# Performance work log

Hardware: AMD Instinct MI355X
Metric: run time of the kernel (lower is better)

The kernel has to match this reference:

```python
import jax, jax.numpy as jnp
import numpy as np

NUM_HEADS = 8
D_MODEL = 128
MAX_LEN = 500  # RelativePositionalEncoding default


def setup_inputs() -> dict:
    key = jax.random.key(0)
    ks = jax.random.split(key, 13)
    B, S, D = 4, 1024, D_MODEL
    d = {
        'query': jax.random.normal(ks[0], (B, S, D), jnp.float32),
        'key': jax.random.normal(ks[1], (B, S, D), jnp.float32),
        'value': jax.random.normal(ks[2], (B, S, D), jnp.float32),
        # nn.Linear weights stored as (out, in), bias (out,)
        'Wq': jax.random.normal(ks[3], (D, D), jnp.float32) * 0.05,
        'bq': jax.random.normal(ks[4], (D,), jnp.float32) * 0.05,
        'Wk': jax.random.normal(ks[5], (D, D), jnp.float32) * 0.05,
        'bk': jax.random.normal(ks[6], (D,), jnp.float32) * 0.05,
        'Wv': jax.random.normal(ks[7], (D, D), jnp.float32) * 0.05,
        'bv': jax.random.normal(ks[8], (D,), jnp.float32) * 0.05,
        'Wo': jax.random.normal(ks[9], (D, D), jnp.float32) * 0.05,
        'bo': jax.random.normal(ks[10], (D,), jnp.float32) * 0.05,
        # embeddings_table: (2*max_len+1, d_model)
        'emb_table': jax.random.normal(ks[11], (2 * MAX_LEN + 1, D), jnp.float32) * 0.05,
    }
    return d


def reference(query, key, value, Wq, bq, Wk, bk, Wv, bv, Wo, bo, emb_table):
    B, S, D = query.shape
    H = NUM_HEADS
    hd = D // H

    def proj(x, W, b):
        # nn.Linear: x @ W.T + b, then split heads -> [B,H,S,hd]
        return (x @ W.T + b).reshape(B, S, H, hd).transpose(0, 2, 1, 3)

    Q = proj(query, Wq, bq)
    K = proj(key, Wk, bk)
    V = proj(value, Wv, bv)

    scores = jnp.einsum('bhqd,bhkd->bhqk', Q, K) / jnp.sqrt(jnp.float32(hd))

    # relative position bias: table gather (S,S,D) -> (S,S,H,hd);
    # batch dim of the torch expand is redundant, so contract directly.
    r = jnp.arange(S)
    rel_idx = jnp.clip(r[None, :] - r[:, None], -MAX_LEN, MAX_LEN) + MAX_LEN  # (S,S)
    E = emb_table[rel_idx].reshape(S, S, H, hd)  # (q,k,h,d)
    scores = scores + jnp.einsum('bhqd,qkhd->bhqk', Q, E)

    attn = jax.nn.softmax(scores + 1e-9, axis=-1)
    out = jnp.einsum('bhqk,bhkd->bhqd', attn, V)
    out = out.transpose(0, 2, 1, 3).reshape(B, S, D)
    return out @ Wo.T + bo
```

## Files before the change

### kernel.cpp

```cpp
#include <hip/hip_runtime.h>

#define NH 8
#define HD 16
#define SLEN 1024
#define BATCH 4
#define MAXL 500
#define NSEG 4
#define KTILES_PER_SEG 8

typedef float f32x4  __attribute__((ext_vector_type(4)));
typedef float f32x16 __attribute__((ext_vector_type(16)));
typedef short s16x8  __attribute__((ext_vector_type(8)));

__device__ inline ushort f2bf(float f) {
    uint u = __builtin_bit_cast(uint, f);
    u = (u + 0x7fffu + ((u >> 16) & 1u)) >> 16;
    return (ushort)u;
}
__device__ inline float bf2f(ushort h) {
    uint u = ((uint)h) << 16;
    return __builtin_bit_cast(float, u);
}

__global__ __launch_bounds__(256) void emb2bf(const float* __restrict__ emb,
                                              ushort* __restrict__ emb_bf)
{
    int idx = blockIdx.x * 256 + threadIdx.x;
    int e0 = idx * 8;
    if (e0 >= (2 * MAXL + 1) * 128) return;
    const float4 a = *(const float4*)&emb[e0];
    const float4 b = *(const float4*)&emb[e0 + 4];
    ushort tmp[8] = {f2bf(a.x), f2bf(a.y), f2bf(a.z), f2bf(a.w),
                     f2bf(b.x), f2bf(b.y), f2bf(b.z), f2bf(b.w)};
    *(s16x8*)&emb_bf[e0] = *(const s16x8*)tmp;
}

__global__ __launch_bounds__(256) void qkv_proj_mfma(
    const float* __restrict__ xq, const float* __restrict__ xk, const float* __restrict__ xv,
    const float* __restrict__ Wq, const float* __restrict__ bq,
    const float* __restrict__ Wk, const float* __restrict__ bk,
    const float* __restrict__ Wv, const float* __restrict__ bv,
    ushort* __restrict__ Qh, ushort* __restrict__ Kh, ushort* __restrict__ Vt)
{
    const int mode = blockIdx.y;
    const float* x  = (mode == 0) ? xq : (mode == 1) ? xk : xv;
    const float* W  = (mode == 0) ? Wq : (mode == 1) ? Wk : Wv;
    const float* bb = (mode == 0) ? bq : (mode == 1) ? bk : bv;

    __shared__ __align__(16) ushort Xs[64][40];
    __shared__ __align__(16) ushort Ws[128][40];

    const int t = threadIdx.x;
    const int wid = t >> 6, lane = t & 63;
    const int m0 = blockIdx.x * 64;

    f32x4 acc[4][2];
    #pragma unroll
    for (int i = 0; i < 4; ++i)
        #pragma unroll
        for (int j = 0; j < 2; ++j)
            #pragma unroll
            for (int r = 0; r < 4; ++r) acc[i][j][r] = 0.f;

    for (int k0 = 0; k0 < 128; k0 += 32) {
        __syncthreads();
        {
            int m = t >> 2, kb = (t & 3) * 8;
            const float* src = &x[(size_t)(m0 + m) * 128 + k0 + kb];
            const float4 a = *(const float4*)src;
            const float4 b4 = *(const float4*)(src + 4);
            ushort tmp[8] = {f2bf(a.x),f2bf(a.y),f2bf(a.z),f2bf(a.w),
                             f2bf(b4.x),f2bf(b4.y),f2bf(b4.z),f2bf(b4.w)};
            *(s16x8*)&Xs[m][kb] = *(const s16x8*)tmp;
        }
        {
            int n = t >> 1, kb = (t & 1) * 16;
            const float* src = &W[(size_t)n * 128 + k0 + kb];
            ushort tmp[16];
            #pragma unroll
            for (int i = 0; i < 16; ++i) tmp[i] = f2bf(src[i]);
            *(s16x8*)&Ws[n][kb]     = *(const s16x8*)&tmp[0];
            *(s16x8*)&Ws[n][kb + 8] = *(const s16x8*)&tmp[8];
        }
        __syncthreads();
        s16x8 af[4], bf[2];
        #pragma unroll
        for (int ms = 0; ms < 4; ++ms)
            af[ms] = *(const s16x8*)&Xs[16*ms + (lane & 15)][8 * (lane >> 4)];
        #pragma unroll
        for (int ns = 0; ns < 2; ++ns)
            bf[ns] = *(const s16x8*)&Ws[32*wid + 16*ns + (lane & 15)][8 * (lane >> 4)];
        #pragma unroll
        for (int ms = 0; ms < 4; ++ms)
            #pragma unroll
            for (int ns = 0; ns < 2; ++ns)
                acc[ms][ns] = __builtin_amdgcn_mfma_f32_16x16x32_bf16(af[ms], bf[ns], acc[ms][ns], 0, 0, 0);
    }

    const float scale = (mode == 1) ? 0.25f : 1.0f;
    const int b = m0 >> 10;
    #pragma unroll
    for (int ns = 0; ns < 2; ++ns) {
        const int n = 32*wid + 16*ns + (lane & 15);
        const int hh = n >> 4, d = n & 15;
        const float bias = bb[n];
        #pragma unroll
        for (int ms = 0; ms < 4; ++ms) {
            if (mode == 2) {
                ushort4 pk;
                pk.x = f2bf(acc[ms][ns][0] + bias);
                pk.y = f2bf(acc[ms][ns][1] + bias);
                pk.z = f2bf(acc[ms][ns][2] + bias);
                pk.w = f2bf(acc[ms][ns][3] + bias);
                int s0 = (m0 & 1023) + 16*ms + (lane >> 4) * 4;
                *(ushort4*)&Vt[((size_t)((b*8 + hh)*16 + d)) * SLEN + s0] = pk;
            } else {
                ushort* dst = (mode == 0) ? Qh : Kh;
                #pragma unroll
                for (int r = 0; r < 4; ++r) {
                    int mm = m0 + 16*ms + (lane >> 4) * 4 + r;
                    int s = mm & 1023;
                    float v = (acc[ms][ns][r] + bias) * scale;
                    dst[((size_t)(b*8 + hh) * SLEN + s) * HD + d] = f2bf(v);
                }
            }
        }
    }
}

__global__ __launch_bounds__(256) void attn_mfma(
    const ushort* __restrict__ Qh, const ushort* __restrict__ Kh,
    const ushort* __restrict__ Vtg, const ushort* __restrict__ emb_bf,
    float* __restrict__ mp, float* __restrict__ lp, float* __restrict__ op)
{
    __shared__ __align__(16) ushort Kt[32][24];
    __shared__ __align__(16) ushort Vt[16][40];
    __shared__ __align__(16) ushort Eb[160][24];
    __shared__ __align__(16) ushort Pl[4][32][40];
    __shared__ __align__(16) ushort Rl[4][64][36];
    __shared__ float scb[4][32];

    const int tid = threadIdx.x;
    const int wid = tid >> 6, lane = tid & 63;
    const int hi = lane >> 5, q = lane & 31;
    const int bh = blockIdx.y, h = bh & 7;
    const int q0b = blockIdx.x * 128;
    const int q0w = q0b + wid * 32;
    const int seg = blockIdx.z;

    const s16x8 qf = *(const s16x8*)&Qh[((size_t)bh * SLEN + q0w + q) * HD + 8 * hi];

    f32x4 o0, o1;
    #pragma unroll
    for (int r = 0; r < 4; ++r) { o0[r] = 0.f; o1[r] = 0.f; }
    float m = -1e30f, l = 0.f;

    for (int kt = seg * KTILES_PER_SEG; kt < (seg + 1) * KTILES_PER_SEG; ++kt) {
        const int k0 = kt * 32;
        __syncthreads();
        {
            int e = tid * 2, r = e >> 4, d0 = e & 15;
            *(ushort2*)&Kt[r][d0] = *(const ushort2*)&Kh[((size_t)bh * SLEN + k0 + r) * HD + d0];
        }
        {
            int d = tid >> 4, kk = (tid & 15) * 2;
            *(ushort2*)&Vt[d][kk] = *(const ushort2*)&Vtg[((size_t)(bh * 16 + d)) * SLEN + k0 + kk];
        }
        {
            const int relbase = k0 - q0b - 127;
            for (int e = tid; e < 160 * 2; e += 256) {
                int r = e >> 1, c8 = (e & 1) * 8;
                int rel = relbase + r;
                rel = rel < -MAXL ? -MAXL : (rel > MAXL ? MAXL : rel);
                *(s16x8*)&Eb[r][c8] =
                    *(const s16x8*)&emb_bf[(size_t)(rel + MAXL) * 128 + h * HD + c8];
            }
        }
        __syncthreads();

        const s16x8 kf = *(const s16x8*)&Kt[q][8 * hi];
        f32x16 sa;
        #pragma unroll
        for (int i = 0; i < 16; ++i) sa[i] = 0.f;
        sa = __builtin_amdgcn_mfma_f32_32x32x16_bf16(kf, qf, sa, 0, 0, 0);

        const int j0w = 96 - 32 * wid;
        #pragma unroll
        for (int st = 0; st < 2; ++st) {
            const s16x8 ef = *(const s16x8*)&Eb[j0w + 32 * st + q][8 * hi];
            f32x16 ra;
            #pragma unroll
            for (int i = 0; i < 16; ++i) ra[i] = 0.f;
            ra = __builtin_amdgcn_mfma_f32_32x32x16_bf16(qf, ef, ra, 0, 0, 0);
            #pragma unroll
            for (int g = 0; g < 4; ++g) {
                ushort4 pk;
                pk.x = f2bf(ra[4*g + 0]); pk.y = f2bf(ra[4*g + 1]);
                pk.z = f2bf(ra[4*g + 2]); pk.w = f2bf(ra[4*g + 3]);
                *(ushort4*)&Rl[wid][32*st + q][8*g + 4*hi] = pk;
            }
        }

        float p[16];
        float tm = -1e30f;
        #pragma unroll
        for (int r = 0; r < 16; ++r) {
            const int krow = (r & 3) + 8 * (r >> 2) + 4 * hi;
            const float bias = bf2f(Rl[wid][krow - q + 31][q]);
            const float s = sa[r] + bias;
            p[r] = s;
            tm = fmaxf(tm, s);
        }
        tm = fmaxf(tm, __shfl_xor(tm, 32));
        const float mn = fmaxf(m, tm);
        const float scf = __expf(m - mn);
        float ls = 0.f;
        #pragma unroll
        for (int r = 0; r < 16; ++r) { p[r] = __expf(p[r] - mn); ls += p[r]; }
        ls += __shfl_xor(ls, 32);
        l = l * scf + ls;
        m = mn;
        scb[wid][q] = scf;

        #pragma unroll
        for (int g = 0; g < 4; ++g) {
            ushort4 pk;
            pk.x = f2bf(p[4*g + 0]); pk.y = f2bf(p[4*g + 1]);
            pk.z = f2bf(p[4*g + 2]); pk.w = f2bf(p[4*g + 3]);
            *(ushort4*)&Pl[wid][q][8*g + 4*hi] = pk;
        }

        const s16x8 vf = *(const s16x8*)&Vt[lane & 15][8 * (lane >> 4)];
        {
            const s16x8 pa = *(const s16x8*)&Pl[wid][lane & 15][8 * (lane >> 4)];
            #pragma unroll
            for (int r = 0; r < 4; ++r) o0[r] *= scb[wid][(lane >> 4) * 4 + r];
            o0 = __builtin_amdgcn_mfma_f32_16x16x32_bf16(pa, vf, o0, 0, 0, 0);
        }
        {
            const s16x8 pa = *(const s16x8*)&Pl[wid][16 + (lane & 15)][8 * (lane >> 4)];
            #pragma unroll
            for (int r = 0; r < 4; ++r) o1[r] *= scb[wid][16 + (lane >> 4) * 4 + r];
            o1 = __builtin_amdgcn_mfma_f32_16x16x32_bf16(pa, vf, o1, 0, 0, 0);
        }
    }

    const size_t pbase = (size_t)(seg * 32 + bh) * SLEN;
    if (hi == 0) {
        mp[pbase + q0w + q] = m;
        lp[pbase + q0w + q] = l;
    }
    #pragma unroll
    for (int half = 0; half < 2; ++half) {
        #pragma unroll
        for (int r = 0; r < 4; ++r) {
            const int qp = half * 16 + (lane >> 4) * 4 + r;
            op[(pbase + q0w + qp) * HD + (lane & 15)] = (half ? o1[r] : o0[r]);
        }
    }
}

__global__ __launch_bounds__(256) void merge_kernel(
    const float* __restrict__ mp, const float* __restrict__ lp,
    const float* __restrict__ op, float* __restrict__ Oh2)
{
    const int idx = blockIdx.x * 256 + threadIdx.x;
    const int d = idx & 15;
    const int row = idx >> 4;
    const int bh = row >> 10, q = row & 1023;
    const int h = bh & 7, b = bh >> 3;

    float ms[NSEG];
    float M = -1e30f;
    #pragma unroll
    for (int s = 0; s < NSEG; ++s) {
        ms[s] = mp[(size_t)s * 32 * SLEN + row];
        M = fmaxf(M, ms[s]);
    }
    float L = 0.f, acc = 0.f;
    #pragma unroll
    for (int s = 0; s < NSEG; ++s) {
        const float w = __expf(ms[s] - M);
        L += lp[(size_t)s * 32 * SLEN + row] * w;
        acc += op[((size_t)s * 32 * SLEN + row) * HD + d] * w;
    }
    Oh2[((size_t)(b * SLEN + q)) * 128 + h * HD + d] = acc / L;
}

__global__ __launch_bounds__(256) void out_proj_mfma(
    const float* __restrict__ x, const float* __restrict__ W, const float* __restrict__ bb,
    float* __restrict__ out)
{
    __shared__ __align__(16) ushort Xs[64][40];
    __shared__ __align__(16) ushort Ws[128][40];

    const int t = threadIdx.x;
    const int wid = t >> 6, lane = t & 63;
    const int m0 = blockIdx.x * 64;

    f32x4 acc[4][2];
    #pragma unroll
    for (int i = 0; i < 4; ++i)
        #pragma unroll
        for (int j = 0; j < 2; ++j)
            #pragma unroll
            for (int r = 0; r < 4; ++r) acc[i][j][r] = 0.f;

    for (int k0 = 0; k0 < 128; k0 += 32) {
        __syncthreads();
        {
            int m = t >> 2, kb = (t & 3) * 8;
            const float* src = &x[(size_t)(m0 + m) * 128 + k0 + kb];
            const float4 a = *(const float4*)src;
            const float4 b4 = *(const float4*)(src + 4);
            ushort tmp[8] = {f2bf(a.x),f2bf(a.y),f2bf(a.z),f2bf(a.w),
                             f2bf(b4.x),f2bf(b4.y),f2bf(b4.z),f2bf(b4.w)};
            *(s16x8*)&Xs[m][kb] = *(const s16x8*)tmp;
        }
        {
            int n = t >> 1, kb = (t & 1) * 16;
            const float* src = &W[(size_t)n * 128 + k0 + kb];
            ushort tmp[16];
            #pragma unroll
            for (int i = 0; i < 16; ++i) tmp[i] = f2bf(src[i]);
            *(s16x8*)&Ws[n][kb]     = *(const s16x8*)&tmp[0];
            *(s16x8*)&Ws[n][kb + 8] = *(const s16x8*)&tmp[8];
        }
        __syncthreads();
        s16x8 af[4], bf[2];
        #pragma unroll
        for (int ms = 0; ms < 4; ++ms)
            af[ms] = *(const s16x8*)&Xs[16*ms + (lane & 15)][8 * (lane >> 4)];
        #pragma unroll
        for (int ns = 0; ns < 2; ++ns)
            bf[ns] = *(const s16x8*)&Ws[32*wid + 16*ns + (lane & 15)][8 * (lane >> 4)];
        #pragma unroll
        for (int ms = 0; ms < 4; ++ms)
            #pragma unroll
            for (int ns = 0; ns < 2; ++ns)
                acc[ms][ns] = __builtin_amdgcn_mfma_f32_16x16x32_bf16(af[ms], bf[ns], acc[ms][ns], 0, 0, 0);
    }

    #pragma unroll
    for (int ns = 0; ns < 2; ++ns) {
        const int n = 32*wid + 16*ns + (lane & 15);
        const float bias = bb[n];
        #pragma unroll
        for (int ms = 0; ms < 4; ++ms)
            #pragma unroll
            for (int r = 0; r < 4; ++r) {
                const int mm = m0 + 16*ms + (lane >> 4) * 4 + r;
                out[(size_t)mm * 128 + n] = acc[ms][ns][r] + bias;
            }
    }
}

extern "C" void kernel_launch(void* const* d_in, const int* in_sizes, int n_in,
                              void* d_out, int out_size, void* d_ws, size_t ws_size,
                              hipStream_t stream)
{
    const float* query  = (const float*)d_in[0];
    const float* key_in = (const float*)d_in[1];
    const float* value  = (const float*)d_in[2];
    const float* Wq = (const float*)d_in[3];
    const float* bq = (const float*)d_in[4];
    const float* Wk = (const float*)d_in[5];
    const float* bk = (const float*)d_in[6];
    const float* Wv = (const float*)d_in[7];
    const float* bv = (const float*)d_in[8];
    const float* Wo = (const float*)d_in[9];
    const float* bo = (const float*)d_in[10];
    const float* emb = (const float*)d_in[11];
    float* out = (float*)d_out;

    const size_t TEN = (size_t)BATCH * NH * SLEN * HD;
    const size_t ROWS = (size_t)32 * SLEN;
    ushort* qh  = (ushort*)d_ws;
    ushort* kh  = qh + TEN;
    ushort* vtg = kh + TEN;
    float*  oh2 = (float*)(vtg + TEN);
    float*  mp  = oh2 + (size_t)4096 * 128;
    float*  lp  = mp + NSEG * ROWS;
    float*  op  = lp + NSEG * ROWS;
    ushort* embbf = (ushort*)(op + NSEG * ROWS * HD);

    emb2bf<<<63, 256, 0, stream>>>(emb, embbf);
    qkv_proj_mfma<<<dim3(64, 3), 256, 0, stream>>>(
        query, key_in, value, Wq, bq, Wk, bk, Wv, bv, qh, kh, vtg);
    attn_mfma<<<dim3(8, 32, NSEG), 256, 0, stream>>>(qh, kh, vtg, embbf, mp, lp, op);
    merge_kernel<<<(32 * SLEN * HD) / 256, 256, 0, stream>>>(mp, lp, op, oh2);
    out_proj_mfma<<<64, 256, 0, stream>>>(oh2, Wo, bo, out);
}
```

Before: 123.3 us.

## Pre-convert inputs and weights to bf16, use LDS-free single-wave projection GEMMs

```diff
diff --git a/kernel.cpp b/kernel.cpp
--- a/kernel.cpp
+++ b/kernel.cpp
@@ -22,106 +22,111 @@
     return __builtin_bit_cast(float, u);
 }
 
-__global__ __launch_bounds__(256) void emb2bf(const float* __restrict__ emb,
-                                              ushort* __restrict__ emb_bf)
-{
-    int idx = blockIdx.x * 256 + threadIdx.x;
-    int e0 = idx * 8;
-    if (e0 >= (2 * MAXL + 1) * 128) return;
-    const float4 a = *(const float4*)&emb[e0];
-    const float4 b = *(const float4*)&emb[e0 + 4];
+__global__ __launch_bounds__(256) void prep_bf16(
+    const float* __restrict__ xq, const float* __restrict__ xk, const float* __restrict__ xv,
+    const float* __restrict__ Wq, const float* __restrict__ Wk,
+    const float* __restrict__ Wv, const float* __restrict__ Wo,
+    const float* __restrict__ emb,
+    ushort* __restrict__ xqb, ushort* __restrict__ xkb, ushort* __restrict__ xvb,
+    ushort* __restrict__ wqb, ushort* __restrict__ wkb,
+    ushort* __restrict__ wvb, ushort* __restrict__ wob,
+    ushort* __restrict__ embb)
+{
+    const int XTOT = 3 * 524288;
+    const int WTOT = 4 * 16384;
+    const int ETOT = (2 * MAXL + 1) * 128;
+    int e0 = (blockIdx.x * 256 + threadIdx.x) * 8;
+    const float* src;
+    ushort* dst;
+    int off;
+    if (e0 < XTOT) {
+        int which = e0 >> 19; off = e0 & 524287;
+        src = which == 0 ? xq : which == 1 ? xk : xv;
+        dst = which == 0 ? xqb : which == 1 ? xkb : xvb;
+    } else if (e0 < XTOT + WTOT) {
+        int t = e0 - XTOT; int which = t >> 14; off = t & 16383;
+        src = which == 0 ? Wq : which == 1 ? Wk : which == 2 ? Wv : Wo;
+        dst = which == 0 ? wqb : which == 1 ? wkb : which == 2 ? wvb : wob;
+    } else if (e0 < XTOT + WTOT + ETOT) {
+        off = e0 - XTOT - WTOT; src = emb; dst = embb;
+    } else {
+        return;
+    }
+    const float4 a = *(const float4*)&src[off];
+    const float4 b = *(const float4*)&src[off + 4];
     ushort tmp[8] = {f2bf(a.x), f2bf(a.y), f2bf(a.z), f2bf(a.w),
                      f2bf(b.x), f2bf(b.y), f2bf(b.z), f2bf(b.w)};
-    *(s16x8*)&emb_bf[e0] = *(const s16x8*)tmp;
-}
-
-__global__ __launch_bounds__(256) void qkv_proj_mfma(
-    const float* __restrict__ xq, const float* __restrict__ xk, const float* __restrict__ xv,
-    const float* __restrict__ Wq, const float* __restrict__ bq,
-    const float* __restrict__ Wk, const float* __restrict__ bk,
-    const float* __restrict__ Wv, const float* __restrict__ bv,
+    *(s16x8*)&dst[off] = *(const s16x8*)tmp;
+}
+
+__global__ __launch_bounds__(64) void qkv_gemm(
+    const ushort* __restrict__ xqb, const ushort* __restrict__ xkb, const ushort* __restrict__ xvb,
+    const ushort* __restrict__ wqb, const ushort* __restrict__ wkb, const ushort* __restrict__ wvb,
+    const float* __restrict__ bq, const float* __restrict__ bk, const float* __restrict__ bv,
     ushort* __restrict__ Qh, ushort* __restrict__ Kh, ushort* __restrict__ Vt)
 {
     const int mode = blockIdx.y;
-    const float* x  = (mode == 0) ? xq : (mode == 1) ? xk : xv;
-    const float* W  = (mode == 0) ? Wq : (mode == 1) ? Wk : Wv;
-    const float* bb = (mode == 0) ? bq : (mode == 1) ? bk : bv;
-
-    __shared__ __align__(16) ushort Xs[64][40];
-    __shared__ __align__(16) ushort Ws[128][40];
-
-    const int t = threadIdx.x;
-    const int wid = t >> 6, lane = t & 63;
-    const int m0 = blockIdx.x * 64;
-
-    f32x4 acc[4][2];
-    #pragma unroll
-    for (int i = 0; i < 4; ++i)
-        #pragma unroll
-        for (int j = 0; j < 2; ++j)
-            #pragma unroll
-            for (int r = 0; r < 4; ++r) acc[i][j][r] = 0.f;
-
-    for (int k0 = 0; k0 < 128; k0 += 32) {
-        __syncthreads();
-        {
-            int m = t >> 2, kb = (t & 3) * 8;
-            const float* src = &x[(size_t)(m0 + m) * 128 + k0 + kb];
-            const float4 a = *(const float4*)src;
-            const float4 b4 = *(const float4*)(src + 4);
-            ushort tmp[8] = {f2bf(a.x),f2bf(a.y),f2bf(a.z),f2bf(a.w),
-                             f2bf(b4.x),f2bf(b4.y),f2bf(b4.z),f2bf(b4.w)};
-            *(s16x8*)&Xs[m][kb] = *(const s16x8*)tmp;
-        }
-        {
-            int n = t >> 1, kb = (t & 1) * 16;
-            const float* src = &W[(size_t)n * 128 + k0 + kb];
-            ushort tmp[16];
-            #pragma unroll
-            for (int i = 0; i < 16; ++i) tmp[i] = f2bf(src[i]);
-            *(s16x8*)&Ws[n][kb]     = *(const s16x8*)&tmp[0];
-            *(s16x8*)&Ws[n][kb + 8] = *(const s16x8*)&tmp[8];
-        }
-        __syncthreads();
-        s16x8 af[4], bf[2];
-        #pragma unroll
-        for (int ms = 0; ms < 4; ++ms)
-            af[ms] = *(const s16x8*)&Xs[16*ms + (lane & 15)][8 * (lane >> 4)];
+    const ushort* X = mode == 0 ? xqb : mode == 1 ? xkb : xvb;
+    const ushort* W = mode == 0 ? wqb : mode == 1 ? wkb : wvb;
+    const float* bb = mode == 0 ? bq : mode == 1 ? bk : bv;
+
+    const int l = threadIdx.x;
+    const int row = l & 15, kh = l >> 4;
+    const int mt = blockIdx.x >> 2, nq = blockIdx.x & 3;
+    const int m0 = mt * 32, n0 = nq * 32;
+
+    s16x8 af[2][4], bfr[2][4];
+    #pragma unroll
+    for (int ms = 0; ms < 2; ++ms)
+        #pragma unroll
+        for (int ki = 0; ki < 4; ++ki)
+            af[ms][ki] = *(const s16x8*)&X[(size_t)(m0 + 16*ms + row) * 128 + 32*ki + 8*kh];
+    #pragma unroll
+    for (int ns = 0; ns < 2; ++ns)
+        #pragma unroll
+        for (int ki = 0; ki < 4; ++ki)
+            bfr[ns][ki] = *(const s16x8*)&W[(size_t)(n0 + 16*ns + row) * 128 + 32*ki + 8*kh];
+
+    f32x4 acc[2][2];
+    #pragma unroll
+    for (int ms = 0; ms < 2; ++ms)
         #pragma unroll
         for (int ns = 0; ns < 2; ++ns)
-            bf[ns] = *(const s16x8*)&Ws[32*wid + 16*ns + (lane & 15)][8 * (lane >> 4)];
-        #pragma unroll
-        for (int ms = 0; ms < 4; ++ms)
+            #pragma unroll
+            for (int r = 0; r < 4; ++r) acc[ms][ns][r] = 0.f;
+
+    #pragma unroll
+    for (int ki = 0; ki < 4; ++ki)
+        #pragma unroll
+        for (int ms = 0; ms < 2; ++ms)
             #pragma unroll
             for (int ns = 0; ns < 2; ++ns)
-                acc[ms][ns] = __builtin_amdgcn_mfma_f32_16x16x32_bf16(af[ms], bf[ns], acc[ms][ns], 0, 0, 0);
-    }
+                acc[ms][ns] = __builtin_amdgcn_mfma_f32_16x16x32_bf16(af[ms][ki], bfr[ns][ki], acc[ms][ns], 0, 0, 0);
 
     const float scale = (mode == 1) ? 0.25f : 1.0f;
     const int b = m0 >> 10;
     #pragma unroll
     for (int ns = 0; ns < 2; ++ns) {
-        const int n = 32*wid + 16*ns + (lane & 15);
+        const int n = n0 + 16*ns + row;
         const int hh = n >> 4, d = n & 15;
         const float bias = bb[n];
         #pragma unroll
-        for (int ms = 0; ms < 4; ++ms) {
+        for (int ms = 0; ms < 2; ++ms) {
             if (mode == 2) {
                 ushort4 pk;
                 pk.x = f2bf(acc[ms][ns][0] + bias);
                 pk.y = f2bf(acc[ms][ns][1] + bias);
                 pk.z = f2bf(acc[ms][ns][2] + bias);
                 pk.w = f2bf(acc[ms][ns][3] + bias);
-                int s0 = (m0 & 1023) + 16*ms + (lane >> 4) * 4;
+                const int s0 = (m0 & 1023) + 16*ms + kh * 4;
                 *(ushort4*)&Vt[((size_t)((b*8 + hh)*16 + d)) * SLEN + s0] = pk;
             } else {
                 ushort* dst = (mode == 0) ? Qh : Kh;
                 #pragma unroll
                 for (int r = 0; r < 4; ++r) {
-                    int mm = m0 + 16*ms + (lane >> 4) * 4 + r;
-                    int s = mm & 1023;
-                    float v = (acc[ms][ns][r] + bias) * scale;
-                    dst[((size_t)(b*8 + hh) * SLEN + s) * HD + d] = f2bf(v);
+                    const int mm = m0 + 16*ms + kh * 4 + r;
+                    const int s = mm & 1023;
+                    dst[((size_t)(b*8 + hh) * SLEN + s) * HD + d] = f2bf((acc[ms][ns][r] + bias) * scale);
                 }
             }
         }
@@ -262,7 +267,7 @@
 
 __global__ __launch_bounds__(256) void merge_kernel(
     const float* __restrict__ mp, const float* __restrict__ lp,
-    const float* __restrict__ op, float* __restrict__ Oh2)
+    const float* __restrict__ op, ushort* __restrict__ ohbf)
 {
     const int idx = blockIdx.x * 256 + threadIdx.x;
     const int d = idx & 15;
@@ -284,72 +289,55 @@
         L += lp[(size_t)s * 32 * SLEN + row] * w;
         acc += op[((size_t)s * 32 * SLEN + row) * HD + d] * w;
     }
-    Oh2[((size_t)(b * SLEN + q)) * 128 + h * HD + d] = acc / L;
-}
-
-__global__ __launch_bounds__(256) void out_proj_mfma(
-    const float* __restrict__ x, const float* __restrict__ W, const float* __restrict__ bb,
-    float* __restrict__ out)
-{
-    __shared__ __align__(16) ushort Xs[64][40];
-    __shared__ __align__(16) ushort Ws[128][40];
-
-    const int t = threadIdx.x;
-    const int wid = t >> 6, lane = t & 63;
-    const int m0 = blockIdx.x * 64;
-
-    f32x4 acc[4][2];
-    #pragma unroll
-    for (int i = 0; i < 4; ++i)
-        #pragma unroll
-        for (int j = 0; j < 2; ++j)
-            #pragma unroll
-            for (int r = 0; r < 4; ++r) acc[i][j][r] = 0.f;
-
-    for (int k0 = 0; k0 < 128; k0 += 32) {
-        __syncthreads();
-        {
-            int m = t >> 2, kb = (t & 3) * 8;
-            const float* src = &x[(size_t)(m0 + m) * 128 + k0 + kb];
-            const float4 a = *(const float4*)src;
-            const float4 b4 = *(const float4*)(src + 4);
-            ushort tmp[8] = {f2bf(a.x),f2bf(a.y),f2bf(a.z),f2bf(a.w),
-                             f2bf(b4.x),f2bf(b4.y),f2bf(b4.z),f2bf(b4.w)};
-            *(s16x8*)&Xs[m][kb] = *(const s16x8*)tmp;
-        }
-        {
-            int n = t >> 1, kb = (t & 1) * 16;
-            const float* src = &W[(size_t)n * 128 + k0 + kb];
-            ushort tmp[16];
-            #pragma unroll
-            for (int i = 0; i < 16; ++i) tmp[i] = f2bf(src[i]);
-            *(s16x8*)&Ws[n][kb]     = *(const s16x8*)&tmp[0];
-            *(s16x8*)&Ws[n][kb + 8] = *(const s16x8*)&tmp[8];
-        }
-        __syncthreads();
-        s16x8 af[4], bf[2];
-        #pragma unroll
-        for (int ms = 0; ms < 4; ++ms)
-            af[ms] = *(const s16x8*)&Xs[16*ms + (lane & 15)][8 * (lane >> 4)];
+    ohbf[((size_t)(b * SLEN + q)) * 128 + h * HD + d] = f2bf(acc / L);
+}
+
+__global__ __launch_bounds__(64) void out_gemm(
+    const ushort* __restrict__ ohbf, const ushort* __restrict__ wob,
+    const float* __restrict__ bo, float* __restrict__ out)
+{
+    const int l = threadIdx.x;
+    const int row = l & 15, kh = l >> 4;
+    const int mt = blockIdx.x >> 2, nq = blockIdx.x & 3;
+    const int m0 = mt * 32, n0 = nq * 32;
+
+    s16x8 af[2][4], bfr[2][4];
+    #pragma unroll
+    for (int ms = 0; ms < 2; ++ms)
+        #pragma unroll
+        for (int ki = 0; ki < 4; ++ki)
+            af[ms][ki] = *(const s16x8*)&ohbf[(size_t)(m0 + 16*ms + row) * 128 + 32*ki + 8*kh];
+    #pragma unroll
+    for (int ns = 0; ns < 2; ++ns)
+        #pragma unroll
+        for (int ki = 0; ki < 4; ++ki)
+            bfr[ns][ki] = *(const s16x8*)&wob[(size_t)(n0 + 16*ns + row) * 128 + 32*ki + 8*kh];
+
+    f32x4 acc[2][2];
+    #pragma unroll
+    for (int ms = 0; ms < 2; ++ms)
         #pragma unroll
         for (int ns = 0; ns < 2; ++ns)
-            bf[ns] = *(const s16x8*)&Ws[32*wid + 16*ns + (lane & 15)][8 * (lane >> 4)];
-        #pragma unroll
-        for (int ms = 0; ms < 4; ++ms)
+            #pragma unroll
+            for (int r = 0; r < 4; ++r) acc[ms][ns][r] = 0.f;
+
+    #pragma unroll
+    for (int ki = 0; ki < 4; ++ki)
+        #pragma unroll
+        for (int ms = 0; ms < 2; ++ms)
             #pragma unroll
             for (int ns = 0; ns < 2; ++ns)
-                acc[ms][ns] = __builtin_amdgcn_mfma_f32_16x16x32_bf16(af[ms], bf[ns], acc[ms][ns], 0, 0, 0);
-    }
+                acc[ms][ns] = __builtin_amdgcn_mfma_f32_16x16x32_bf16(af[ms][ki], bfr[ns][ki], acc[ms][ns], 0, 0, 0);
 
     #pragma unroll
     for (int ns = 0; ns < 2; ++ns) {
-        const int n = 32*wid + 16*ns + (lane & 15);
-        const float bias = bb[n];
-        #pragma unroll
-        for (int ms = 0; ms < 4; ++ms)
+        const int n = n0 + 16*ns + row;
+        const float bias = bo[n];
+        #pragma unroll
+        for (int ms = 0; ms < 2; ++ms)
             #pragma unroll
             for (int r = 0; r < 4; ++r) {
-                const int mm = m0 + 16*ms + (lane >> 4) * 4 + r;
+                const int mm = m0 + 16*ms + kh * 4 + r;
                 out[(size_t)mm * 128 + n] = acc[ms][ns][r] + bias;
             }
     }
@@ -374,20 +362,31 @@
     float* out = (float*)d_out;
 
     const size_t TEN = (size_t)BATCH * NH * SLEN * HD;
+    const size_t WE  = 16384;
+    const size_t EE  = (size_t)(2 * MAXL + 1) * 128;
     const size_t ROWS = (size_t)32 * SLEN;
-    ushort* qh  = (ushort*)d_ws;
-    ushort* kh  = qh + TEN;
-    ushort* vtg = kh + TEN;
-    float*  oh2 = (float*)(vtg + TEN);
-    float*  mp  = oh2 + (size_t)4096 * 128;
-    float*  lp  = mp + NSEG * ROWS;
-    float*  op  = lp + NSEG * ROWS;
-    ushort* embbf = (ushort*)(op + NSEG * ROWS * HD);
-
-    emb2bf<<<63, 256, 0, stream>>>(emb, embbf);
-    qkv_proj_mfma<<<dim3(64, 3), 256, 0, stream>>>(
-        query, key_in, value, Wq, bq, Wk, bk, Wv, bv, qh, kh, vtg);
-    attn_mfma<<<dim3(8, 32, NSEG), 256, 0, stream>>>(qh, kh, vtg, embbf, mp, lp, op);
-    merge_kernel<<<(32 * SLEN * HD) / 256, 256, 0, stream>>>(mp, lp, op, oh2);
-    out_proj_mfma<<<64, 256, 0, stream>>>(oh2, Wo, bo, out);
-}
+
+    ushort* qh   = (ushort*)d_ws;
+    ushort* kh   = qh + TEN;
+    ushort* vtg  = kh + TEN;
+    ushort* xqb  = vtg + TEN;
+    ushort* xkb  = xqb + TEN;
+    ushort* xvb  = xkb + TEN;
+    ushort* wqb  = xvb + TEN;
+    ushort* wkb  = wqb + WE;
+    ushort* wvb  = wkb + WE;
+    ushort* wob  = wvb + WE;
+    ushort* embb = wob + WE;
+    ushort* ohbf = embb + EE;
+    float*  mp   = (float*)(ohbf + TEN);
+    float*  lp   = mp + NSEG * ROWS;
+    float*  op   = lp + NSEG * ROWS;
+
+    prep_bf16<<<863, 256, 0, stream>>>(query, key_in, value, Wq, Wk, Wv, Wo, emb,
+                                       xqb, xkb, xvb, wqb, wkb, wvb, wob, embb);
+    qkv_gemm<<<dim3(512, 3), 64, 0, stream>>>(xqb, xkb, xvb, wqb, wkb, wvb,
+                                              bq, bk, bv, qh, kh, vtg);
+    attn_mfma<<<dim3(8, 32, NSEG), 256, 0, stream>>>(qh, kh, vtg, embb, mp, lp, op);
+    merge_kernel<<<(32 * SLEN * HD) / 256, 256, 0, stream>>>(mp, lp, op, ohbf);
+    out_gemm<<<512, 64, 0, stream>>>(ohbf, wob, bo, out);
+}
```

Measured after the change: 120.2 us. 1.03x faster.
